# Kernel optimization log

Measured on AMD Instinct MI355X. Metric: run time of the kernel, lower is better.

## Reference

```python
import jax, jax.numpy as jnp
import numpy as np

N = 100000
E = 1600000
D_IN = 128
D_OUT = 64


def setup_inputs() -> dict:
    key = jax.random.key(0)
    k1, k2, k3, k4, k5 = jax.random.split(key, 5)
    x = jax.random.normal(k1, (N, D_IN), dtype=jnp.float32)
    edge_row = jax.random.randint(k2, (E,), 0, N, dtype=jnp.int32)
    edge_col = jax.random.randint(k3, (E,), 0, N, dtype=jnp.int32)
    edge_val = jax.random.uniform(k4, (E,), dtype=jnp.float32)
    # Glorot-uniform init as in the torch module
    init_range = np.sqrt(6.0 / (D_IN + D_OUT))
    weight = jax.random.uniform(k5, (D_IN, D_OUT), dtype=jnp.float32,
                                minval=-init_range, maxval=init_range)
    return {"x": x, "edge_row": edge_row, "edge_col": edge_col,
            "edge_val": edge_val, "weight": weight}


def reference(x, edge_row, edge_col, edge_val, weight):
    # Dense projection: [N, D_in] @ [D_in, D_out] -> [N, D_out]
    xw = jnp.matmul(x, weight)
    # Sparse aggregation (SpMM with COO support): out[r] += val * xw[c]
    msgs = edge_val[:, None] * xw[edge_col]          # [E, D_out]
    out = jax.ops.segment_sum(msgs, edge_row, num_segments=x.shape[0])
    # bias=False, activation=relu
    return jax.nn.relu(out)
```

## Files before the change

kernel.cpp:

```cpp
#include <hip/hip_runtime.h>

#define NN 100000
#define DIN 128
#define DOUT 64
#define NE 1600000

#define BSHIFT 7
#define BROWS 128
#define NBB 783
#define NBP 1024
#define CAP 2560
#define QRN 5
#define EPB 4096
#define NBLK 391

#define XWB_B  0u
#define GCUR_B 12800000u
#define BPAD_B (GCUR_B + 8192u)
#define WS_NEED (BPAD_B + (unsigned)NBB * CAP * 8u)

typedef unsigned short u16;
typedef unsigned int u32;
typedef __attribute__((ext_vector_type(8))) short v8s;
typedef __attribute__((ext_vector_type(4))) float v4f;

__device__ __forceinline__ float bf2f(u16 u) {
  return __uint_as_float(((u32)u) << 16);
}
__device__ __forceinline__ u16 f2bf(float f) {
  u32 x = __float_as_uint(f);
  u32 r = x + 0x7fffu + ((x >> 16) & 1u);
  return (u16)(r >> 16);
}

__global__ __launch_bounds__(256) void gemm_kernel(
    const float* __restrict__ x, const float* __restrict__ w,
    u16* __restrict__ xwb, int* __restrict__ gz) {
  if (gz != nullptr && threadIdx.x == 0 && blockIdx.x < NBB)
    gz[blockIdx.x] = 0;

  __shared__ u16 wlds[16 * 64 * 8];
  const int t = threadIdx.x;
  const int lane = t & 63;
  const int wv = t >> 6;

  #pragma unroll
  for (int pi = 0; pi < 4; ++pi) {
    const int p = t * 4 + pi;
    const int f = p >> 6, lp = p & 63;
    const int kc = f >> 2, nc = f & 3;
    const int kg = lp >> 4, lr = lp & 15;
    const int kbase = kc * 32 + kg * 8;
    u32 pk[4];
    #pragma unroll
    for (int h = 0; h < 4; ++h) {
      const u32 lo = f2bf(w[(kbase + 2 * h)     * DOUT + nc * 16 + lr]);
      const u32 hi = f2bf(w[(kbase + 2 * h + 1) * DOUT + nc * 16 + lr]);
      pk[h] = lo | (hi << 16);
    }
    *reinterpret_cast<uint4*>(&wlds[p * 8]) =
        make_uint4(pk[0], pk[1], pk[2], pk[3]);
  }
  __syncthreads();

  const int row0 = blockIdx.x * 64 + wv * 16;
  if (row0 >= NN) return;
  const int lrow = lane & 15;
  const int lkg  = lane >> 4;

  v8s Bf[4][4];
  #pragma unroll
  for (int kc = 0; kc < 4; ++kc)
    #pragma unroll
    for (int nc = 0; nc < 4; ++nc)
      Bf[kc][nc] = *reinterpret_cast<const v8s*>(
          &wlds[((kc * 4 + nc) * 64 + lane) * 8]);

  const float* xr = x + (size_t)(row0 + lrow) * DIN + lkg * 8;
  float4 xa[4][2];
  #pragma unroll
  for (int kc = 0; kc < 4; ++kc) {
    xa[kc][0] = *reinterpret_cast<const float4*>(xr + kc * 32);
    xa[kc][1] = *reinterpret_cast<const float4*>(xr + kc * 32 + 4);
  }

  v4f acc[4];
  #pragma unroll
  for (int nc = 0; nc < 4; ++nc) acc[nc] = (v4f){0.f, 0.f, 0.f, 0.f};

  #pragma unroll
  for (int kc = 0; kc < 4; ++kc) {
    v8s Af;
    Af[0] = (short)f2bf(xa[kc][0].x);
    Af[1] = (short)f2bf(xa[kc][0].y);
    Af[2] = (short)f2bf(xa[kc][0].z);
    Af[3] = (short)f2bf(xa[kc][0].w);
    Af[4] = (short)f2bf(xa[kc][1].x);
    Af[5] = (short)f2bf(xa[kc][1].y);
    Af[6] = (short)f2bf(xa[kc][1].z);
    Af[7] = (short)f2bf(xa[kc][1].w);
    #pragma unroll
    for (int nc = 0; nc < 4; ++nc)
      acc[nc] = __builtin_amdgcn_mfma_f32_16x16x32_bf16(Af, Bf[kc][nc],
                                                        acc[nc], 0, 0, 0);
  }

  #pragma unroll
  for (int nc = 0; nc < 4; ++nc)
    #pragma unroll
    for (int j = 0; j < 4; ++j)
      xwb[(size_t)(row0 + lkg * 4 + j) * DOUT + nc * 16 + lrow] =
          f2bf(acc[nc][j]);
}

__global__ __launch_bounds__(512) void place5_kernel(
    const int* __restrict__ erow, const int* __restrict__ ecol,
    const float* __restrict__ eval_, int* __restrict__ gcur,
    int2* __restrict__ bpad) {
  __shared__ int  hist[NBP];
  __shared__ int  lofs[NBP];
  __shared__ int  lcur[NBP];
  __shared__ int  base_[NBP];
  __shared__ int  wtot[8];
  __shared__ u16  sb[EPB];
  __shared__ int2 dstl[EPB];

  const int t = threadIdx.x;
  const int lane = t & 63;
  const int wv = t >> 6;
  const int e0 = blockIdx.x * EPB;
  const int e1 = min(e0 + EPB, NE);
  const int ecount = e1 - e0;

  hist[t] = 0;        hist[t + 512] = 0;
  lcur[t] = 0;        lcur[t + 512] = 0;
  __syncthreads();

  int er[8], ec[8];
  float ev[8];
  #pragma unroll
  for (int k = 0; k < 8; ++k) {
    const int e = e0 + t + k * 512;
    if (e < e1) {
      er[k] = erow[e];
      ec[k] = ecol[e];
      ev[k] = eval_[e];
      atomicAdd(&hist[er[k] >> BSHIFT], 1);
    } else {
      er[k] = -1;
    }
  }
  __syncthreads();

  const int ha = hist[2 * t], hb = hist[2 * t + 1];
  const int ps = ha + hb;
  int s = ps;
  #pragma unroll
  for (int o = 1; o < 64; o <<= 1) {
    const int u = __shfl_up(s, o);
    if (lane >= o) s += u;
  }
  if (lane == 63) wtot[wv] = s;
  __syncthreads();
  int woff = 0;
  #pragma unroll
  for (int w = 0; w < 8; ++w) woff += (w < wv) ? wtot[w] : 0;
  const int excl = woff + s - ps;
  lofs[2 * t]     = excl;
  lofs[2 * t + 1] = excl + ha;
  #pragma unroll
  for (int i = t; i < NBP; i += 512) {
    const int h = hist[i];
    base_[i] = (h && i < NBB) ? atomicAdd(&gcur[i], h) : 0;
  }
  __syncthreads();

  #pragma unroll
  for (int k = 0; k < 8; ++k) {
    if (er[k] >= 0) {
      const int b = er[k] >> BSHIFT;
      const int pos = lofs[b] + atomicAdd(&lcur[b], 1);
      dstl[pos] = make_int2(((er[k] & (BROWS - 1)) << 17) | ec[k],
                            __float_as_int(ev[k]));
      sb[pos] = (u16)b;
    }
  }
  __syncthreads();

  for (int p = t; p < ecount; p += 512) {
    const int b = sb[p];
    const int rk = base_[b] + (p - lofs[b]);
    if (rk < CAP) bpad[(long)b * CAP + rk] = dstl[p];
  }
}

__global__ __launch_bounds__(512) void agg7_kernel(
    const int* __restrict__ gcur, const int2* __restrict__ bpad,
    const u16* __restrict__ xwb, float* __restrict__ out) {
  __shared__ int2 dst[CAP];
  __shared__ int  hist[BROWS];
  __shared__ int  lptr[BROWS + 1];
  __shared__ int  cur[BROWS];

  const int bucket = blockIdx.x;
  const int t = threadIdx.x;
  const int count = min(gcur[bucket], CAP);
  const long sbase = (long)bucket * CAP;

  if (t < BROWS) hist[t] = 0;
  __syncthreads();

  int2 qr[QRN];
  #pragma unroll
  for (int k = 0; k < QRN; ++k) {
    const int e = t + k * 512;
    qr[k].x = -1;
    if (e < count) {
      qr[k] = bpad[sbase + e];
      atomicAdd(&hist[(qr[k].x >> 17) & (BROWS - 1)], 1);
    }
  }
  __syncthreads();

  if (t < 64) {
    const int h0 = hist[2 * t], h1 = hist[2 * t + 1];
    const int ps = h0 + h1;
    int s = ps;
    #pragma unroll
    for (int o = 1; o < 64; o <<= 1) {
      const int u = __shfl_up(s, o);
      if (t >= o) s += u;
    }
    const int excl = s - ps;
    lptr[2 * t]     = excl;        cur[2 * t]     = excl;
    lptr[2 * t + 1] = excl + h0;   cur[2 * t + 1] = excl + h0;
    if (t == 63) lptr[BROWS] = s;
  }
  __syncthreads();

  #pragma unroll
  for (int k = 0; k < QRN; ++k) {
    if (qr[k].x >= 0) {
      const int r = (qr[k].x >> 17) & (BROWS - 1);
      const int pos = atomicAdd(&cur[r], 1);
      dst[pos] = qr[k];
    }
  }
  __syncthreads();

  const int lane = t & 63;
  const int wave = t >> 6;
  const int slot = lane >> 4;
  const int li   = lane & 15;
  const int row0 = bucket << BSHIFT;
  const int cmax = count - 1;

  for (int r = wave; r < BROWS; r += 8) {
    const int row = row0 + r;
    if (row >= NN) break;
    const int s = lptr[r], en = lptr[r + 1];
    float a0 = 0.f, a1 = 0.f, a2 = 0.f, a3 = 0.f;
    for (int e = s; e < en; e += 8) {
      {
        const int idx = e + slot;
        const int2 q = dst[min(idx, cmax)];
        const float v = (idx < en) ? __int_as_float(q.y) : 0.f;
        const u32 col = (u32)q.x & 0x1FFFFu;
        const uint2 g = *reinterpret_cast<const uint2*>(
            xwb + (size_t)col * DOUT + li * 4);
        a0 = fmaf(v, __uint_as_float(g.x << 16), a0);
        a1 = fmaf(v, __uint_as_float(g.x & 0xFFFF0000u), a1);
        a2 = fmaf(v, __uint_as_float(g.y << 16), a2);
        a3 = fmaf(v, __uint_as_float(g.y & 0xFFFF0000u), a3);
      }
      {
        const int idx = e + 4 + slot;
        const int2 q = dst[min(idx, cmax)];
        const float v = (idx < en) ? __int_as_float(q.y) : 0.f;
        const u32 col = (u32)q.x & 0x1FFFFu;
        const uint2 g = *reinterpret_cast<const uint2*>(
            xwb + (size_t)col * DOUT + li * 4);
        a0 = fmaf(v, __uint_as_float(g.x << 16), a0);
        a1 = fmaf(v, __uint_as_float(g.x & 0xFFFF0000u), a1);
        a2 = fmaf(v, __uint_as_float(g.y << 16), a2);
        a3 = fmaf(v, __uint_as_float(g.y & 0xFFFF0000u), a3);
      }
    }
    a0 += __shfl_xor(a0, 16); a0 += __shfl_xor(a0, 32);
    a1 += __shfl_xor(a1, 16); a1 += __shfl_xor(a1, 32);
    a2 += __shfl_xor(a2, 16); a2 += __shfl_xor(a2, 32);
    a3 += __shfl_xor(a3, 16); a3 += __shfl_xor(a3, 32);
    if (slot == 0) {
      float4 o;
      o.x = fmaxf(a0, 0.f); o.y = fmaxf(a1, 0.f);
      o.z = fmaxf(a2, 0.f); o.w = fmaxf(a3, 0.f);
      *reinterpret_cast<float4*>(&out[(size_t)row * DOUT + li * 4]) = o;
    }
  }
}

__global__ __launch_bounds__(256) void scatter_kernel(
    const int* __restrict__ erow, const int* __restrict__ ecol,
    const float* __restrict__ eval_, const u16* __restrict__ xwb,
    float* __restrict__ out) {
  const int wave = (blockIdx.x * blockDim.x + threadIdx.x) >> 6;
  const int lane = threadIdx.x & 63;
  const int nwaves = (gridDim.x * blockDim.x) >> 6;
  const int per = (NE + nwaves - 1) / nwaves;
  const int e0 = wave * per;
  const int e1 = min(e0 + per, NE);
  for (int base = e0; base < e1; base += 64) {
    const int e = base + lane;
    int r = 0, c = 0; float v = 0.f;
    if (e < e1) { r = erow[e]; c = ecol[e]; v = eval_[e]; }
    const int cnt = min(64, e1 - base);
    for (int j = 0; j < cnt; ++j) {
      const int rj = __shfl(r, j);
      const int cj = __shfl(c, j);
      const float vj = __shfl(v, j);
      atomicAdd(&out[rj * DOUT + lane], vj * bf2f(xwb[cj * DOUT + lane]));
    }
  }
}

__global__ __launch_bounds__(256) void finish_kernel(float* __restrict__ out) {
  const int idx = (blockIdx.x * blockDim.x + threadIdx.x) * 4;
  if (idx < NN * DOUT) {
    float4 a = *reinterpret_cast<const float4*>(&out[idx]);
    a.x = fmaxf(a.x, 0.f); a.y = fmaxf(a.y, 0.f);
    a.z = fmaxf(a.z, 0.f); a.w = fmaxf(a.w, 0.f);
    *reinterpret_cast<float4*>(&out[idx]) = a;
  }
}

extern "C" void kernel_launch(void* const* d_in, const int* in_sizes, int n_in,
                              void* d_out, int out_size, void* d_ws, size_t ws_size,
                              hipStream_t stream) {
  const float* x     = (const float*)d_in[0];
  const int*   erow  = (const int*)d_in[1];
  const int*   ecol  = (const int*)d_in[2];
  const float* eval_ = (const float*)d_in[3];
  const float* w     = (const float*)d_in[4];
  float* out = (float*)d_out;

  char* ws = (char*)d_ws;
  u16* xwb = (u16*)(ws + XWB_B);
  const bool big_ws = (ws_size >= (size_t)WS_NEED);
  int* gcur = big_ws ? (int*)(ws + GCUR_B) : nullptr;

  const int gemm_grid = (NN + 63) / 64;
  gemm_kernel<<<gemm_grid, 256, 0, stream>>>(x, w, xwb, gcur);

  if (big_ws) {
    int2* bpad = (int2*)(ws + BPAD_B);
    place5_kernel<<<NBLK, 512, 0, stream>>>(erow, ecol, eval_, gcur, bpad);
    agg7_kernel<<<NBB, 512, 0, stream>>>(gcur, bpad, xwb, out);
  } else {
    hipMemsetAsync(d_out, 0, (size_t)NN * DOUT * sizeof(float), stream);
    scatter_kernel<<<2048, 256, 0, stream>>>(erow, ecol, eval_, xwb, out);
    const int fin_grid = (NN * DOUT / 4 + 255) / 256;
    finish_kernel<<<fin_grid, 256, 0, stream>>>(out);
  }
}
```

Baseline: 71.89 us.

## Fuse GEMM and edge bucketing into one heterogeneous kernel launch

```diff
diff --git a/kernel.cpp b/kernel.cpp
--- a/kernel.cpp
+++ b/kernel.cpp
@@ -13,12 +13,21 @@
 #define QRN 5
 #define EPB 4096
 #define NBLK 391
+#define GBLK 782
 
 #define XWB_B  0u
 #define GCUR_B 12800000u
 #define BPAD_B (GCUR_B + 8192u)
 #define WS_NEED (BPAD_B + (unsigned)NBB * CAP * 8u)
 
+#define SM_DSTL 0u
+#define SM_SB   32768u
+#define SM_HIST 40960u
+#define SM_LOFS 45056u
+#define SM_LCUR 49152u
+#define SM_WTOT 53248u
+#define SM_BYTES 53280u
+
 typedef unsigned short u16;
 typedef unsigned int u32;
 typedef __attribute__((ext_vector_type(8))) short v8s;
@@ -33,20 +42,98 @@
   return (u16)(r >> 16);
 }
 
-__global__ __launch_bounds__(256) void gemm_kernel(
+__global__ __launch_bounds__(512, 4) void fused_gp_kernel(
     const float* __restrict__ x, const float* __restrict__ w,
-    u16* __restrict__ xwb, int* __restrict__ gz) {
-  if (gz != nullptr && threadIdx.x == 0 && blockIdx.x < NBB)
-    gz[blockIdx.x] = 0;
-
-  __shared__ u16 wlds[16 * 64 * 8];
+    u16* __restrict__ xwb,
+    const int* __restrict__ erow, const int* __restrict__ ecol,
+    const float* __restrict__ eval_, int* __restrict__ gcur,
+    int2* __restrict__ bpad) {
+  __shared__ __align__(16) char smem[SM_BYTES];
   const int t = threadIdx.x;
   const int lane = t & 63;
   const int wv = t >> 6;
 
-  #pragma unroll
-  for (int pi = 0; pi < 4; ++pi) {
-    const int p = t * 4 + pi;
+  if (blockIdx.x < NBLK) {
+    int2* dstl = (int2*)(smem + SM_DSTL);
+    u16*  sb   = (u16*)(smem + SM_SB);
+    int*  hist = (int*)(smem + SM_HIST);
+    int*  lofs = (int*)(smem + SM_LOFS);
+    int*  lcur = (int*)(smem + SM_LCUR);
+    int*  wtot = (int*)(smem + SM_WTOT);
+
+    const int e0 = blockIdx.x * EPB;
+    const int e1 = min(e0 + EPB, NE);
+    const int ecount = e1 - e0;
+
+    hist[t] = 0;        hist[t + 512] = 0;
+    lcur[t] = 0;        lcur[t + 512] = 0;
+    __syncthreads();
+
+    int er[8], ec[8];
+    float ev[8];
+    #pragma unroll
+    for (int k = 0; k < 8; ++k) {
+      const int e = e0 + t + k * 512;
+      if (e < e1) {
+        er[k] = erow[e];
+        ec[k] = ecol[e];
+        ev[k] = eval_[e];
+        atomicAdd(&hist[er[k] >> BSHIFT], 1);
+      } else {
+        er[k] = -1;
+      }
+    }
+    __syncthreads();
+
+    const int ha = hist[2 * t], hb = hist[2 * t + 1];
+    const int ps = ha + hb;
+    int s = ps;
+    #pragma unroll
+    for (int o = 1; o < 64; o <<= 1) {
+      const int u = __shfl_up(s, o);
+      if (lane >= o) s += u;
+    }
+    if (lane == 63) wtot[wv] = s;
+    __syncthreads();
+    int woff = 0;
+    #pragma unroll
+    for (int w8 = 0; w8 < 8; ++w8) woff += (w8 < wv) ? wtot[w8] : 0;
+    const int excl = woff + s - ps;
+    lofs[2 * t]     = excl;
+    lofs[2 * t + 1] = excl + ha;
+    #pragma unroll
+    for (int i = t; i < NBP; i += 512) {
+      const int h = hist[i];
+      hist[i] = (h && i < NBB) ? atomicAdd(&gcur[i], h) : 0;
+    }
+    __syncthreads();
+
+    #pragma unroll
+    for (int k = 0; k < 8; ++k) {
+      if (er[k] >= 0) {
+        const int b = er[k] >> BSHIFT;
+        const int pos = lofs[b] + atomicAdd(&lcur[b], 1);
+        dstl[pos] = make_int2(((er[k] & (BROWS - 1)) << 17) | ec[k],
+                              __float_as_int(ev[k]));
+        sb[pos] = (u16)b;
+      }
+    }
+    __syncthreads();
+
+    for (int p = t; p < ecount; p += 512) {
+      const int b = sb[p];
+      const int rk = hist[b] + (p - lofs[b]);
+      if (rk < CAP) bpad[(long)b * CAP + rk] = dstl[p];
+    }
+    return;
+  }
+
+  u16* wlds = (u16*)smem;
+  const int gb = blockIdx.x - NBLK;
+
+  #pragma unroll
+  for (int pi = 0; pi < 2; ++pi) {
+    const int p = t * 2 + pi;
     const int f = p >> 6, lp = p & 63;
     const int kc = f >> 2, nc = f & 3;
     const int kg = lp >> 4, lr = lp & 15;
@@ -63,7 +150,7 @@
   }
   __syncthreads();
 
-  const int row0 = blockIdx.x * 64 + wv * 16;
+  const int row0 = gb * 128 + wv * 16;
   if (row0 >= NN) return;
   const int lrow = lane & 15;
   const int lkg  = lane >> 4;
@@ -111,87 +198,6 @@
     for (int j = 0; j < 4; ++j)
       xwb[(size_t)(row0 + lkg * 4 + j) * DOUT + nc * 16 + lrow] =
           f2bf(acc[nc][j]);
-}
-
-__global__ __launch_bounds__(512) void place5_kernel(
-    const int* __restrict__ erow, const int* __restrict__ ecol,
-    const float* __restrict__ eval_, int* __restrict__ gcur,
-    int2* __restrict__ bpad) {
-  __shared__ int  hist[NBP];
-  __shared__ int  lofs[NBP];
-  __shared__ int  lcur[NBP];
-  __shared__ int  base_[NBP];
-  __shared__ int  wtot[8];
-  __shared__ u16  sb[EPB];
-  __shared__ int2 dstl[EPB];
-
-  const int t = threadIdx.x;
-  const int lane = t & 63;
-  const int wv = t >> 6;
-  const int e0 = blockIdx.x * EPB;
-  const int e1 = min(e0 + EPB, NE);
-  const int ecount = e1 - e0;
-
-  hist[t] = 0;        hist[t + 512] = 0;
-  lcur[t] = 0;        lcur[t + 512] = 0;
-  __syncthreads();
-
-  int er[8], ec[8];
-  float ev[8];
-  #pragma unroll
-  for (int k = 0; k < 8; ++k) {
-    const int e = e0 + t + k * 512;
-    if (e < e1) {
-      er[k] = erow[e];
-      ec[k] = ecol[e];
-      ev[k] = eval_[e];
-      atomicAdd(&hist[er[k] >> BSHIFT], 1);
-    } else {
-      er[k] = -1;
-    }
-  }
-  __syncthreads();
-
-  const int ha = hist[2 * t], hb = hist[2 * t + 1];
-  const int ps = ha + hb;
-  int s = ps;
-  #pragma unroll
-  for (int o = 1; o < 64; o <<= 1) {
-    const int u = __shfl_up(s, o);
-    if (lane >= o) s += u;
-  }
-  if (lane == 63) wtot[wv] = s;
-  __syncthreads();
-  int woff = 0;
-  #pragma unroll
-  for (int w = 0; w < 8; ++w) woff += (w < wv) ? wtot[w] : 0;
-  const int excl = woff + s - ps;
-  lofs[2 * t]     = excl;
-  lofs[2 * t + 1] = excl + ha;
-  #pragma unroll
-  for (int i = t; i < NBP; i += 512) {
-    const int h = hist[i];
-    base_[i] = (h && i < NBB) ? atomicAdd(&gcur[i], h) : 0;
-  }
-  __syncthreads();
-
-  #pragma unroll
-  for (int k = 0; k < 8; ++k) {
-    if (er[k] >= 0) {
-      const int b = er[k] >> BSHIFT;
-      const int pos = lofs[b] + atomicAdd(&lcur[b], 1);
-      dstl[pos] = make_int2(((er[k] & (BROWS - 1)) << 17) | ec[k],
-                            __float_as_int(ev[k]));
-      sb[pos] = (u16)b;
-    }
-  }
-  __syncthreads();
-
-  for (int p = t; p < ecount; p += 512) {
-    const int b = sb[p];
-    const int rk = base_[b] + (p - lofs[b]);
-    if (rk < CAP) bpad[(long)b * CAP + rk] = dstl[p];
-  }
 }
 
 __global__ __launch_bounds__(512) void agg7_kernel(
@@ -299,6 +305,83 @@
   }
 }
 
+__global__ __launch_bounds__(256) void gemm_kernel(
+    const float* __restrict__ x, const float* __restrict__ w,
+    u16* __restrict__ xwb) {
+  __shared__ u16 wlds[16 * 64 * 8];
+  const int t = threadIdx.x;
+  const int lane = t & 63;
+  const int wv = t >> 6;
+
+  #pragma unroll
+  for (int pi = 0; pi < 4; ++pi) {
+    const int p = t * 4 + pi;
+    const int f = p >> 6, lp = p & 63;
+    const int kc = f >> 2, nc = f & 3;
+    const int kg = lp >> 4, lr = lp & 15;
+    const int kbase = kc * 32 + kg * 8;
+    u32 pk[4];
+    #pragma unroll
+    for (int h = 0; h < 4; ++h) {
+      const u32 lo = f2bf(w[(kbase + 2 * h)     * DOUT + nc * 16 + lr]);
+      const u32 hi = f2bf(w[(kbase + 2 * h + 1) * DOUT + nc * 16 + lr]);
+      pk[h] = lo | (hi << 16);
+    }
+    *reinterpret_cast<uint4*>(&wlds[p * 8]) =
+        make_uint4(pk[0], pk[1], pk[2], pk[3]);
+  }
+  __syncthreads();
+
+  const int row0 = blockIdx.x * 64 + wv * 16;
+  if (row0 >= NN) return;
+  const int lrow = lane & 15;
+  const int lkg  = lane >> 4;
+
+  v8s Bf[4][4];
+  #pragma unroll
+  for (int kc = 0; kc < 4; ++kc)
+    #pragma unroll
+    for (int nc = 0; nc < 4; ++nc)
+      Bf[kc][nc] = *reinterpret_cast<const v8s*>(
+          &wlds[((kc * 4 + nc) * 64 + lane) * 8]);
+
+  const float* xr = x + (size_t)(row0 + lrow) * DIN + lkg * 8;
+  float4 xa[4][2];
+  #pragma unroll
+  for (int kc = 0; kc < 4; ++kc) {
+    xa[kc][0] = *reinterpret_cast<const float4*>(xr + kc * 32);
+    xa[kc][1] = *reinterpret_cast<const float4*>(xr + kc * 32 + 4);
+  }
+
+  v4f acc[4];
+  #pragma unroll
+  for (int nc = 0; nc < 4; ++nc) acc[nc] = (v4f){0.f, 0.f, 0.f, 0.f};
+
+  #pragma unroll
+  for (int kc = 0; kc < 4; ++kc) {
+    v8s Af;
+    Af[0] = (short)f2bf(xa[kc][0].x);
+    Af[1] = (short)f2bf(xa[kc][0].y);
+    Af[2] = (short)f2bf(xa[kc][0].z);
+    Af[3] = (short)f2bf(xa[kc][0].w);
+    Af[4] = (short)f2bf(xa[kc][1].x);
+    Af[5] = (short)f2bf(xa[kc][1].y);
+    Af[6] = (short)f2bf(xa[kc][1].z);
+    Af[7] = (short)f2bf(xa[kc][1].w);
+    #pragma unroll
+    for (int nc = 0; nc < 4; ++nc)
+      acc[nc] = __builtin_amdgcn_mfma_f32_16x16x32_bf16(Af, Bf[kc][nc],
+                                                        acc[nc], 0, 0, 0);
+  }
+
+  #pragma unroll
+  for (int nc = 0; nc < 4; ++nc)
+    #pragma unroll
+    for (int j = 0; j < 4; ++j)
+      xwb[(size_t)(row0 + lkg * 4 + j) * DOUT + nc * 16 + lrow] =
+          f2bf(acc[nc][j]);
+}
+
 __global__ __launch_bounds__(256) void scatter_kernel(
     const int* __restrict__ erow, const int* __restrict__ ecol,
     const float* __restrict__ eval_, const u16* __restrict__ xwb,
@@ -345,17 +428,17 @@
 
   char* ws = (char*)d_ws;
   u16* xwb = (u16*)(ws + XWB_B);
-  const bool big_ws = (ws_size >= (size_t)WS_NEED);
-  int* gcur = big_ws ? (int*)(ws + GCUR_B) : nullptr;
-
-  const int gemm_grid = (NN + 63) / 64;
-  gemm_kernel<<<gemm_grid, 256, 0, stream>>>(x, w, xwb, gcur);
-
-  if (big_ws) {
+
+  if (ws_size >= (size_t)WS_NEED) {
+    int*  gcur = (int*)(ws + GCUR_B);
     int2* bpad = (int2*)(ws + BPAD_B);
-    place5_kernel<<<NBLK, 512, 0, stream>>>(erow, ecol, eval_, gcur, bpad);
+
+    hipMemsetAsync(gcur, 0, NBB * 4, stream);
+    fused_gp_kernel<<<NBLK + GBLK, 512, 0, stream>>>(
+        x, w, xwb, erow, ecol, eval_, gcur, bpad);
     agg7_kernel<<<NBB, 512, 0, stream>>>(gcur, bpad, xwb, out);
   } else {
+    gemm_kernel<<<(NN + 63) / 64, 256, 0, stream>>>(x, w, xwb);
     hipMemsetAsync(d_out, 0, (size_t)NN * DOUT * sizeof(float), stream);
     scatter_kernel<<<2048, 256, 0, stream>>>(erow, ecol, eval_, xwb, out);
     const int fin_grid = (NN * DOUT / 4 + 255) / 256;
```

Measured after the change: 74.58 us. 3.7% more time.
